# Performance work log

Hardware: AMD Instinct MI355X
Metric: run time of the kernel (lower is better)

The kernel has to match this reference:

```python
import jax, jax.numpy as jnp
import numpy as np

INPUT_SIZE = (224, 224)


def setup_inputs() -> dict:
    key = jax.random.key(0)
    k1, k2, k3 = jax.random.split(key, 3)
    feat2 = jax.random.normal(k1, (16, 512, 28, 28), dtype=jnp.float32)
    feat3 = jax.random.normal(k2, (16, 1024, 14, 14), dtype=jnp.float32)
    memory_bank = jax.random.normal(k3, (16384, 1536), dtype=jnp.float32)
    return {"feat2": feat2, "feat3": feat3, "memory_bank": memory_bank}


def reference(feat2, feat3, memory_bank):
    b, c2, h, w = feat2.shape
    c3 = feat3.shape[1]
    # interpolate(feat3, size=(h,w), mode='bilinear', align_corners=False)
    feat3_up = jax.image.resize(feat3, (b, c3, h, w), method='bilinear')
    features = jnp.concatenate([feat2, feat3_up], axis=1)  # [b, c, h, w]
    c = c2 + c3
    feats = features.transpose(0, 2, 3, 1).reshape(-1, c)  # [N, c]
    x_sq = jnp.sum(feats * feats, axis=1, keepdims=True)            # [N, 1]
    m_sq = jnp.sum(memory_bank * memory_bank, axis=1)[None, :]      # [1, M]
    d2 = x_sq + m_sq - 2.0 * (feats @ memory_bank.T)                # [N, M]
    min_d = jnp.sqrt(jnp.maximum(jnp.min(d2, axis=1), 0.0))         # [N]
    anomaly_map = min_d.reshape(b, 1, h, w)
    anomaly_map = jax.image.resize(
        anomaly_map, (b, 1, INPUT_SIZE[0], INPUT_SIZE[1]), method='bilinear')
    pred_score = jnp.max(anomaly_map.reshape(b, -1), axis=1)
    return anomaly_map, pred_score
```

## Files before the change

### kernel.cpp

```cpp
#include <hip/hip_runtime.h>
#include <math.h>

#define N_ROWS 12544
#define C_DIM  1536
#define M_ROWS 16384
#define BATCH  16

#define QS    16.0f
#define S2x2  0.0078125f
#define S2    0.00390625f

typedef int   i32x4 __attribute__((ext_vector_type(4)));
typedef unsigned char u8;
typedef signed char   i8;

__device__ __forceinline__ unsigned fkey(float f) {
  unsigned u = __float_as_uint(f);
  return (u & 0x80000000u) ? ~u : (u | 0x80000000u);
}
__device__ __forceinline__ float funkey(unsigned k) {
  unsigned u = (k & 0x80000000u) ? (k ^ 0x80000000u) : ~k;
  return __uint_as_float(u);
}

__device__ __forceinline__ void gl_lds16(const void* g, void* l) {
  __builtin_amdgcn_global_load_lds(
      (__attribute__((address_space(1))) void*)(g),
      (__attribute__((address_space(3))) void*)(l), 16, 0, 0);
}

__device__ __forceinline__ int quant(float v) {
  int q = __float2int_rn(v * QS);
  return max(-127, min(127, q));
}

#define FSTRIDE 1552

__global__ __launch_bounds__(512) void prep_all(
    const float* __restrict__ feat2, const float* __restrict__ feat3,
    const float* __restrict__ mb,
    i8* __restrict__ feats, i8* __restrict__ mbb,
    float* __restrict__ xsq, float* __restrict__ msq,
    unsigned* __restrict__ dmin, unsigned* __restrict__ score) {
  const int blk = blockIdx.x;
  const int t = threadIdx.x;
  __shared__ float sred[8];
  __shared__ u8 fsm[28 * FSTRIDE];
  __shared__ int sxq[28];

  if (blk < M_ROWS) {
    const int j = blk;
    const float* in = mb + (size_t)j * C_DIM;
    i8* outp = mbb + (size_t)j * C_DIM;
    float ssq = 0.f;
    if (t < 384) {
      const float4 v = *(const float4*)(in + t * 4);
      int q0 = quant(v.x), q1 = quant(v.y), q2 = quant(v.z), q3 = quant(v.w);
      unsigned w = (unsigned)(q0 & 0xFF) | ((unsigned)(q1 & 0xFF) << 8)
                 | ((unsigned)(q2 & 0xFF) << 16) | ((unsigned)(q3 & 0xFF) << 24);
      *(unsigned*)(outp + t * 4) = w;
      ssq = (float)(q0*q0 + q1*q1 + q2*q2 + q3*q3);
    }
    for (int off = 32; off > 0; off >>= 1) ssq += __shfl_down(ssq, off, 64);
    if ((t & 63) == 0) sred[t >> 6] = ssq;
    __syncthreads();
    if (t == 0) {
      float s = 0.f;
#pragma unroll
      for (int wv = 0; wv < 6; wv++) s += sred[wv];
      msq[j] = S2 * s;
    }
    if (blk == 0 && t < BATCH) score[t] = 0u;
  } else {
    const int f = blk - M_ROWS;
    const int b = f / 28, y = f % 28;
    const int n0 = b * 784 + y * 28;

    const float sy = 0.5f * y - 0.25f;
    const int y0 = (int)floorf(sy); const float fy = sy - (float)y0;
    const int y0c = max(y0, 0), y1c = min(y0 + 1, 13);
    const float wy0 = 1.f - fy, wy1 = fy;

    const int g  = t >> 5;
    const int l2 = t & 31;
    const float sx = 0.5f * l2 - 0.25f;
    const int x0 = (int)floorf(sx); const float fx = sx - (float)x0;
    const int x0c = max(x0, 0), x1c = min(x0 + 1, 13);
    const float wx0 = 1.f - fx, wx1 = fx;

    if (t < 28) sxq[t] = 0;

    const float* f2b = feat2 + (size_t)b * 512 * 784 + y * 28;
#pragma unroll 4
    for (int i = 0; i < 32; i++) {
      const int c = i * 16 + g;
      if (l2 < 28) {
        float v = f2b[(size_t)c * 784 + l2];
        fsm[l2 * FSTRIDE + c] = (u8)(i8)quant(v);
      }
    }

    const float* f3b = feat3 + (size_t)b * 1024 * 196;
#pragma unroll 4
    for (int i = 0; i < 64; i++) {
      const int cc = i * 16 + g;
      const float* f3 = f3b + (size_t)cc * 196;
      float v = 0.f;
      if (l2 < 14)       v = f3[y0c * 14 + l2];
      else if (l2 < 28)  v = f3[y1c * 14 + (l2 - 14)];
      float t0 = wy0 * __shfl(v, x0c, 32)      + wy1 * __shfl(v, 14 + x0c, 32);
      float t1 = wy0 * __shfl(v, x1c, 32)      + wy1 * __shfl(v, 14 + x1c, 32);
      if (l2 < 28) {
        float o = wx0 * t0 + wx1 * t1;
        fsm[l2 * FSTRIDE + 512 + cc] = (u8)(i8)quant(o);
      }
    }
    __syncthreads();

    i8* orow = feats + (size_t)n0 * C_DIM;
    for (int idx = t; idx < 28 * 96; idx += 512) {
      const int row = idx / 96, col = idx % 96;
      i32x4 wv = *(const i32x4*)(fsm + row * FSTRIDE + col * 16);
      *(i32x4*)(orow + (size_t)row * C_DIM + col * 16) = wv;
      int s = 0;
#pragma unroll
      for (int k = 0; k < 4; k++) {
        const int w = wv[k];
        const int b0 = (int)(i8)(w & 0xFF), b1 = (int)(i8)((w >> 8) & 0xFF);
        const int b2 = (int)(i8)((w >> 16) & 0xFF), b3 = (int)(i8)(w >> 24);
        s += b0*b0 + b1*b1 + b2*b2 + b3*b3;
      }
      atomicAdd(&sxq[row], s);
    }
    __syncthreads();
    if (t < 28) {
      xsq[n0 + t] = S2 * (float)sxq[t];
      dmin[n0 + t] = 0xFFFFFFFFu;
    }
  }
}

__global__ void gemm_min(const i8* __restrict__ X, const i8* __restrict__ Mb,
                         const float* __restrict__ msq,
                         unsigned* __restrict__ dmin) {
  __shared__ u8 As[16384];
  __shared__ u8 Bs[16384];
  __shared__ unsigned smin[128];
  const int t = threadIdx.x;
  const int mtile = blockIdx.x;
  const int ntile = blockIdx.y;
  const int lane = t & 63, wave = t >> 6;
  const int wm = wave >> 1, wn = wave & 1;
  if (t < 128) smin[t] = 0xFFFFFFFFu;

  const int row0 = ntile * 128;
  const int col0 = mtile * 128;
  const int s_row = t >> 2;
  const int s_ch  = (t & 3) ^ ((t >> 3) & 3);
  const i8* ga = X  + (size_t)(row0 + s_row) * C_DIM + s_ch * 16;
  const i8* gb = Mb + (size_t)(col0 + s_row) * C_DIM + s_ch * 16;
  u8* la = As + t * 16;
  u8* lb = Bs + t * 16;

  i32x4 acc[4][4];
  const i32x4 zero = {0, 0, 0, 0};
#pragma unroll
  for (int mi = 0; mi < 4; mi++)
#pragma unroll
    for (int ni = 0; ni < 4; ni++) acc[mi][ni] = zero;

  const int quad = lane >> 4, l16 = lane & 15;
  const int fsw = (l16 >> 1) & 3;
  const int slot = ((quad ^ fsw) * 16);
  const u8* arow = As + (wm * 64 + l16) * 64 + slot;
  const u8* brow = Bs + (wn * 64 + l16) * 64 + slot;

  for (int k0 = 0; k0 < C_DIM; k0 += 128) {
    __syncthreads();
    gl_lds16(ga + k0,                    la);
    gl_lds16(ga + 64 * C_DIM + k0,       la + 4096);
    gl_lds16(ga + k0 + 64,               la + 8192);
    gl_lds16(ga + 64 * C_DIM + k0 + 64,  la + 12288);
    gl_lds16(gb + k0,                    lb);
    gl_lds16(gb + 64 * C_DIM + k0,       lb + 4096);
    gl_lds16(gb + k0 + 64,               lb + 8192);
    gl_lds16(gb + 64 * C_DIM + k0 + 64,  lb + 12288);
    __syncthreads();
#pragma unroll
    for (int sub = 0; sub < 2; sub++) {
      i32x4 af[4], bf[4];
#pragma unroll
      for (int mi = 0; mi < 4; mi++)
        af[mi] = *(const i32x4*)(arow + sub * 8192 + mi * 1024);
#pragma unroll
      for (int ni = 0; ni < 4; ni++)
        bf[ni] = *(const i32x4*)(brow + sub * 8192 + ni * 1024);
#pragma unroll
      for (int mi = 0; mi < 4; mi++)
#pragma unroll
        for (int ni = 0; ni < 4; ni++)
          acc[mi][ni] = __builtin_amdgcn_mfma_i32_16x16x64_i8(
              af[mi], bf[ni], acc[mi][ni], 0, 0, 0);
    }
  }

  float msql[4];
#pragma unroll
  for (int ni = 0; ni < 4; ni++)
    msql[ni] = msq[col0 + wn * 64 + ni * 16 + l16];

#pragma unroll
  for (int mi = 0; mi < 4; mi++) {
#pragma unroll
    for (int r = 0; r < 4; r++) {
      float v = msql[0] - S2x2 * (float)acc[mi][0][r];
#pragma unroll
      for (int ni = 1; ni < 4; ni++)
        v = fminf(v, msql[ni] - S2x2 * (float)acc[mi][ni][r]);
      v = fminf(v, __shfl_xor(v, 1, 64));
      v = fminf(v, __shfl_xor(v, 2, 64));
      v = fminf(v, __shfl_xor(v, 4, 64));
      v = fminf(v, __shfl_xor(v, 8, 64));
      if (l16 == 0) {
        int lrow = wm * 64 + mi * 16 + quad * 4 + r;
        atomicMin(&smin[lrow], fkey(v));
      }
    }
  }
  __syncthreads();
  if (t < 128) atomicMin(&dmin[row0 + t], smin[t]);
}

__global__ void finalize(const unsigned* __restrict__ dmin,
                         const float* __restrict__ xsq,
                         float* __restrict__ out) {
  const int b = blockIdx.x, slice = blockIdx.y, t = threadIdx.x;
  __shared__ float smap[784];
  __shared__ float sred[4];
  for (int i = t; i < 784; i += 256) {
    float d2 = xsq[b * 784 + i] + funkey(dmin[b * 784 + i]);
    smap[i] = sqrtf(fmaxf(d2, 0.f));
  }
  __syncthreads();
  float* omap = out + (size_t)b * 50176;
  float tmax = 0.f;
  const int p0 = slice * 6272;
  for (int p = p0 + t; p < p0 + 6272; p += 256) {
    const int Y = p / 224, Xp = p % 224;
    const float sy = Y * 0.125f - 0.4375f;
    const float sx = Xp * 0.125f - 0.4375f;
    const int y0 = (int)floorf(sy); const float fy = sy - (float)y0;
    const int x0 = (int)floorf(sx); const float fx = sx - (float)x0;
    const int y0c = max(y0, 0), y1c = min(y0 + 1, 27);
    const int x0c = max(x0, 0), x1c = min(x0 + 1, 27);
    float v = (1.f-fy)*((1.f-fx)*smap[y0c*28+x0c] + fx*smap[y0c*28+x1c])
            +      fy *((1.f-fx)*smap[y1c*28+x0c] + fx*smap[y1c*28+x1c]);
    omap[p] = v;
    tmax = fmaxf(tmax, v);
  }
  for (int off = 32; off > 0; off >>= 1)
    tmax = fmaxf(tmax, __shfl_down(tmax, off, 64));
  if ((t & 63) == 0) sred[t >> 6] = tmax;
  __syncthreads();
  if (t == 0) {
    float m = fmaxf(fmaxf(sred[0], sred[1]), fmaxf(sred[2], sred[3]));
    atomicMax((unsigned*)(out + 802816 + b), __float_as_uint(m));
  }
}

extern "C" void kernel_launch(void* const* d_in, const int* in_sizes, int n_in,
                              void* d_out, int out_size, void* d_ws, size_t ws_size,
                              hipStream_t stream) {
  const float* feat2 = (const float*)d_in[0];
  const float* feat3 = (const float*)d_in[1];
  const float* mb    = (const float*)d_in[2];
  char* ws = (char*)d_ws;
  i8*       feats = (i8*)ws;
  i8*       mbb   = (i8*)(ws + 19267584);
  float*    xsq   = (float*)(ws + 44433408);
  float*    msq   = (float*)(ws + 44483584);
  unsigned* dmin  = (unsigned*)(ws + 44549120);
  float* out = (float*)d_out;

  prep_all<<<M_ROWS + 448, 512, 0, stream>>>(
      feat2, feat3, mb, feats, mbb, xsq, msq, dmin,
      (unsigned*)(out + 802816));
  gemm_min<<<dim3(128, 98), 256, 0, stream>>>(feats, mbb, msq, dmin);
  finalize<<<dim3(BATCH, 8), 256, 0, stream>>>(dmin, xsq, out);
}
```

Measured before the change: 532.1 us.

## Enlarge GEMM tile to 256x128 with XCD-aware block mapping; batch memory-bank quantization

The int8 GEMM tile grows from 128x128 to 256x128, so each wave holds 8x4 MFMA accumulators. This doubles reuse of B tiles loaded into LDS and halves the number of blocks. A 1-D grid with an XCD-aware swizzle keeps blocks that share the same memory-bank column tiles on one XCD, aiming at better L2 locality. The prep kernel now quantizes 4 memory-bank rows per 512-thread block, using all threads instead of 384 per row, and feature blocks are moved to the front of the grid. The larger tile raises VGPR use and LDS to 48KB, which may reduce occupancy.

```diff
diff --git a/kernel.cpp b/kernel.cpp
--- a/kernel.cpp
+++ b/kernel.cpp
@@ -48,32 +48,29 @@
   __shared__ u8 fsm[28 * FSTRIDE];
   __shared__ int sxq[28];
 
-  if (blk < M_ROWS) {
-    const int j = blk;
-    const float* in = mb + (size_t)j * C_DIM;
-    i8* outp = mbb + (size_t)j * C_DIM;
+  if (blk >= 448) {
+    const int j0 = (blk - 448) * 4;
+    const int r = t >> 7, j = t & 127;
+    const int row = j0 + r;
+    const float* in = mb + (size_t)row * C_DIM;
+    i8* outp = mbb + (size_t)row * C_DIM;
     float ssq = 0.f;
-    if (t < 384) {
-      const float4 v = *(const float4*)(in + t * 4);
+#pragma unroll
+    for (int i = 0; i < 3; i++) {
+      const int f4 = j + 128 * i;
+      const float4 v = *(const float4*)(in + f4 * 4);
       int q0 = quant(v.x), q1 = quant(v.y), q2 = quant(v.z), q3 = quant(v.w);
       unsigned w = (unsigned)(q0 & 0xFF) | ((unsigned)(q1 & 0xFF) << 8)
                  | ((unsigned)(q2 & 0xFF) << 16) | ((unsigned)(q3 & 0xFF) << 24);
-      *(unsigned*)(outp + t * 4) = w;
-      ssq = (float)(q0*q0 + q1*q1 + q2*q2 + q3*q3);
+      *(unsigned*)(outp + f4 * 4) = w;
+      ssq += (float)(q0*q0 + q1*q1 + q2*q2 + q3*q3);
     }
     for (int off = 32; off > 0; off >>= 1) ssq += __shfl_down(ssq, off, 64);
     if ((t & 63) == 0) sred[t >> 6] = ssq;
     __syncthreads();
-    if (t == 0) {
-      float s = 0.f;
-#pragma unroll
-      for (int wv = 0; wv < 6; wv++) s += sred[wv];
-      msq[j] = S2 * s;
-    }
-    if (blk == 0 && t < BATCH) score[t] = 0u;
+    if (t < 4) msq[j0 + t] = S2 * (sred[2 * t] + sred[2 * t + 1]);
   } else {
-    const int f = blk - M_ROWS;
-    const int b = f / 28, y = f % 28;
+    const int b = blk / 28, y = blk % 28;
     const int n0 = b * 784 + y * 28;
 
     const float sy = 0.5f * y - 0.25f;
@@ -137,24 +134,27 @@
       xsq[n0 + t] = S2 * (float)sxq[t];
       dmin[n0 + t] = 0xFFFFFFFFu;
     }
-  }
-}
-
-__global__ void gemm_min(const i8* __restrict__ X, const i8* __restrict__ Mb,
-                         const float* __restrict__ msq,
-                         unsigned* __restrict__ dmin) {
-  __shared__ u8 As[16384];
+    if (blk == 0 && t < BATCH) score[t] = 0u;
+  }
+}
+
+__global__ __launch_bounds__(256) void gemm_min(
+    const i8* __restrict__ X, const i8* __restrict__ Mb,
+    const float* __restrict__ msq, unsigned* __restrict__ dmin) {
+  __shared__ u8 As[32768];
   __shared__ u8 Bs[16384];
-  __shared__ unsigned smin[128];
+  __shared__ unsigned smin[256];
   const int t = threadIdx.x;
-  const int mtile = blockIdx.x;
-  const int ntile = blockIdx.y;
   const int lane = t & 63, wave = t >> 6;
   const int wm = wave >> 1, wn = wave & 1;
-  if (t < 128) smin[t] = 0xFFFFFFFFu;
-
-  const int row0 = ntile * 128;
+  const int bid = blockIdx.x;
+  const int xcd = bid & 7, per = bid >> 3;
+  const int mtile = (xcd << 4) | (per & 15);
+  const int ntile = per >> 4;
+  const int row0 = ntile * 256;
   const int col0 = mtile * 128;
+  smin[t] = 0xFFFFFFFFu;
+
   const int s_row = t >> 2;
   const int s_ch  = (t & 3) ^ ((t >> 3) & 3);
   const i8* ga = X  + (size_t)(row0 + s_row) * C_DIM + s_ch * 16;
@@ -162,41 +162,45 @@
   u8* la = As + t * 16;
   u8* lb = Bs + t * 16;
 
-  i32x4 acc[4][4];
+  i32x4 acc[8][4];
   const i32x4 zero = {0, 0, 0, 0};
 #pragma unroll
-  for (int mi = 0; mi < 4; mi++)
+  for (int mi = 0; mi < 8; mi++)
 #pragma unroll
     for (int ni = 0; ni < 4; ni++) acc[mi][ni] = zero;
 
   const int quad = lane >> 4, l16 = lane & 15;
   const int fsw = (l16 >> 1) & 3;
   const int slot = ((quad ^ fsw) * 16);
-  const u8* arow = As + (wm * 64 + l16) * 64 + slot;
-  const u8* brow = Bs + (wn * 64 + l16) * 64 + slot;
+  const u8* arow = As + (wm * 128 + l16) * 64 + slot;
+  const u8* brow = Bs + (wn * 64  + l16) * 64 + slot;
 
   for (int k0 = 0; k0 < C_DIM; k0 += 128) {
     __syncthreads();
-    gl_lds16(ga + k0,                    la);
-    gl_lds16(ga + 64 * C_DIM + k0,       la + 4096);
-    gl_lds16(ga + k0 + 64,               la + 8192);
-    gl_lds16(ga + 64 * C_DIM + k0 + 64,  la + 12288);
-    gl_lds16(gb + k0,                    lb);
-    gl_lds16(gb + 64 * C_DIM + k0,       lb + 4096);
-    gl_lds16(gb + k0 + 64,               lb + 8192);
-    gl_lds16(gb + 64 * C_DIM + k0 + 64,  lb + 12288);
+    gl_lds16(ga + k0,                     la);
+    gl_lds16(ga + 64  * C_DIM + k0,       la + 4096);
+    gl_lds16(ga + 128 * C_DIM + k0,       la + 8192);
+    gl_lds16(ga + 192 * C_DIM + k0,       la + 12288);
+    gl_lds16(ga + k0 + 64,                la + 16384);
+    gl_lds16(ga + 64  * C_DIM + k0 + 64,  la + 20480);
+    gl_lds16(ga + 128 * C_DIM + k0 + 64,  la + 24576);
+    gl_lds16(ga + 192 * C_DIM + k0 + 64,  la + 28672);
+    gl_lds16(gb + k0,                     lb);
+    gl_lds16(gb + 64  * C_DIM + k0,       lb + 4096);
+    gl_lds16(gb + k0 + 64,                lb + 8192);
+    gl_lds16(gb + 64  * C_DIM + k0 + 64,  lb + 12288);
     __syncthreads();
 #pragma unroll
     for (int sub = 0; sub < 2; sub++) {
-      i32x4 af[4], bf[4];
-#pragma unroll
-      for (int mi = 0; mi < 4; mi++)
-        af[mi] = *(const i32x4*)(arow + sub * 8192 + mi * 1024);
+      i32x4 af[8], bf[4];
+#pragma unroll
+      for (int mi = 0; mi < 8; mi++)
+        af[mi] = *(const i32x4*)(arow + sub * 16384 + mi * 1024);
 #pragma unroll
       for (int ni = 0; ni < 4; ni++)
         bf[ni] = *(const i32x4*)(brow + sub * 8192 + ni * 1024);
 #pragma unroll
-      for (int mi = 0; mi < 4; mi++)
+      for (int mi = 0; mi < 8; mi++)
 #pragma unroll
         for (int ni = 0; ni < 4; ni++)
           acc[mi][ni] = __builtin_amdgcn_mfma_i32_16x16x64_i8(
@@ -210,7 +214,7 @@
     msql[ni] = msq[col0 + wn * 64 + ni * 16 + l16];
 
 #pragma unroll
-  for (int mi = 0; mi < 4; mi++) {
+  for (int mi = 0; mi < 8; mi++) {
 #pragma unroll
     for (int r = 0; r < 4; r++) {
       float v = msql[0] - S2x2 * (float)acc[mi][0][r];
@@ -222,13 +226,12 @@
       v = fminf(v, __shfl_xor(v, 4, 64));
       v = fminf(v, __shfl_xor(v, 8, 64));
       if (l16 == 0) {
-        int lrow = wm * 64 + mi * 16 + quad * 4 + r;
-        atomicMin(&smin[lrow], fkey(v));
+        atomicMin(&smin[wm * 128 + mi * 16 + quad * 4 + r], fkey(v));
       }
     }
   }
   __syncthreads();
-  if (t < 128) atomicMin(&dmin[row0 + t], smin[t]);
+  atomicMin(&dmin[row0 + t], smin[t]);
 }
 
 __global__ void finalize(const unsigned* __restrict__ dmin,
@@ -282,9 +285,9 @@
   unsigned* dmin  = (unsigned*)(ws + 44549120);
   float* out = (float*)d_out;
 
-  prep_all<<<M_ROWS + 448, 512, 0, stream>>>(
+  prep_all<<<448 + 4096, 512, 0, stream>>>(
       feat2, feat3, mb, feats, mbb, xsq, msq, dmin,
       (unsigned*)(out + 802816));
-  gemm_min<<<dim3(128, 98), 256, 0, stream>>>(feats, mbb, msq, dmin);
+  gemm_min<<<6272, 256, 0, stream>>>(feats, mbb, msq, dmin);
   finalize<<<dim3(BATCH, 8), 256, 0, stream>>>(dmin, xsq, out);
 }
```

Result: slower. 909.4 us (+70.9%).

## Remap GEMM tiles per XCD for L2 reuse and repack memory-bank quantization

Applied to the files above, without the earlier changes.

The GEMM grid is flattened and block IDs are remapped so that each XCD (assigned round-robin by block ID) handles a contiguous set of 16 memory-bank column tiles, which improves L2 reuse of the B operand on the chiplet. The memory-bank quantization now gives one wave per row, eight rows per block, with a wave-only reduction instead of LDS plus a syncthreads. The prep blocks are reordered so the feature blocks come first, and the score reset moves into the feature branch. The mapping assumes the hardware places blocks on XCDs round-robin by block ID.

```diff
diff --git a/kernel.cpp b/kernel.cpp
--- a/kernel.cpp
+++ b/kernel.cpp
@@ -44,36 +44,29 @@
     unsigned* __restrict__ dmin, unsigned* __restrict__ score) {
   const int blk = blockIdx.x;
   const int t = threadIdx.x;
-  __shared__ float sred[8];
   __shared__ u8 fsm[28 * FSTRIDE];
   __shared__ int sxq[28];
 
-  if (blk < M_ROWS) {
-    const int j = blk;
-    const float* in = mb + (size_t)j * C_DIM;
-    i8* outp = mbb + (size_t)j * C_DIM;
+  if (blk >= 448) {
+    const int wave = t >> 6, lane = t & 63;
+    const int row = (blk - 448) * 8 + wave;
+    const float* in = mb + (size_t)row * C_DIM;
+    i8* outp = mbb + (size_t)row * C_DIM;
     float ssq = 0.f;
-    if (t < 384) {
-      const float4 v = *(const float4*)(in + t * 4);
+#pragma unroll
+    for (int i = 0; i < 6; i++) {
+      const int f4 = lane + 64 * i;
+      const float4 v = *(const float4*)(in + f4 * 4);
       int q0 = quant(v.x), q1 = quant(v.y), q2 = quant(v.z), q3 = quant(v.w);
       unsigned w = (unsigned)(q0 & 0xFF) | ((unsigned)(q1 & 0xFF) << 8)
                  | ((unsigned)(q2 & 0xFF) << 16) | ((unsigned)(q3 & 0xFF) << 24);
-      *(unsigned*)(outp + t * 4) = w;
-      ssq = (float)(q0*q0 + q1*q1 + q2*q2 + q3*q3);
+      *(unsigned*)(outp + f4 * 4) = w;
+      ssq += (float)(q0*q0 + q1*q1 + q2*q2 + q3*q3);
     }
     for (int off = 32; off > 0; off >>= 1) ssq += __shfl_down(ssq, off, 64);
-    if ((t & 63) == 0) sred[t >> 6] = ssq;
-    __syncthreads();
-    if (t == 0) {
-      float s = 0.f;
-#pragma unroll
-      for (int wv = 0; wv < 6; wv++) s += sred[wv];
-      msq[j] = S2 * s;
-    }
-    if (blk == 0 && t < BATCH) score[t] = 0u;
+    if (lane == 0) msq[row] = S2 * ssq;
   } else {
-    const int f = blk - M_ROWS;
-    const int b = f / 28, y = f % 28;
+    const int b = blk / 28, y = blk % 28;
     const int n0 = b * 784 + y * 28;
 
     const float sy = 0.5f * y - 0.25f;
@@ -137,18 +130,21 @@
       xsq[n0 + t] = S2 * (float)sxq[t];
       dmin[n0 + t] = 0xFFFFFFFFu;
     }
-  }
-}
-
-__global__ void gemm_min(const i8* __restrict__ X, const i8* __restrict__ Mb,
-                         const float* __restrict__ msq,
-                         unsigned* __restrict__ dmin) {
+    if (blk == 0 && t < BATCH) score[t] = 0u;
+  }
+}
+
+__global__ __launch_bounds__(256) void gemm_min(
+    const i8* __restrict__ X, const i8* __restrict__ Mb,
+    const float* __restrict__ msq, unsigned* __restrict__ dmin) {
   __shared__ u8 As[16384];
   __shared__ u8 Bs[16384];
   __shared__ unsigned smin[128];
   const int t = threadIdx.x;
-  const int mtile = blockIdx.x;
-  const int ntile = blockIdx.y;
+  const int bid = blockIdx.x;
+  const int xcd = bid & 7, per = bid >> 3;
+  const int mtile = (xcd << 4) | (per & 15);
+  const int ntile = per >> 4;
   const int lane = t & 63, wave = t >> 6;
   const int wm = wave >> 1, wn = wave & 1;
   if (t < 128) smin[t] = 0xFFFFFFFFu;
@@ -282,9 +278,9 @@
   unsigned* dmin  = (unsigned*)(ws + 44549120);
   float* out = (float*)d_out;
 
-  prep_all<<<M_ROWS + 448, 512, 0, stream>>>(
+  prep_all<<<448 + 2048, 512, 0, stream>>>(
       feat2, feat3, mb, feats, mbb, xsq, msq, dmin,
       (unsigned*)(out + 802816));
-  gemm_min<<<dim3(128, 98), 256, 0, stream>>>(feats, mbb, msq, dmin);
+  gemm_min<<<12544, 256, 0, stream>>>(feats, mbb, msq, dmin);
   finalize<<<dim3(BATCH, 8), 256, 0, stream>>>(dmin, xsq, out);
 }
```

After: 517.5 us. -2.8%, faster.
